# Kernel optimization log

Measured on AMD Instinct MI355X. Metric: run time of the kernel, lower is better.

## Reference

```python
import jax, jax.numpy as jnp
import numpy as np

B, S, W = 16, 256, 128            # batch, seq_len (word pieces), words per sentence
V, H, L, NH, DH, FF, C = 30522, 768, 12, 12, 64, 3072, 425
EPS = 1e-12                        # HF Bert LayerNorm eps


def setup_inputs() -> dict:
    key = jax.random.key(0)
    kiter = iter(jax.random.split(key, 64))
    nk = lambda: next(kiter)
    # each word maps to 1 or 2 word-pieces -> total pieces in [W, 2W] <= S
    word_piece_tracked = jax.random.randint(nk(), (B, W), 1, 3)
    lengths = jnp.sum(word_piece_tracked, axis=1)
    encoded_batch = jax.random.randint(nk(), (B, S), 0, V)
    mask = (jnp.arange(S)[None, :] < lengths[:, None]).astype(jnp.int32)
    p = lambda *shape: jax.random.normal(nk(), shape, jnp.float32) * 0.02
    return dict(
        encoded_batch=encoded_batch, mask=mask, word_piece_tracked=word_piece_tracked,
        word_emb=p(V, H), pos_emb=p(S, H), type_emb=p(1, H),
        emb_ln_s=jnp.ones((H,), jnp.float32), emb_ln_b=jnp.zeros((H,), jnp.float32),
        Wq=p(L, H, H), bq=p(L, H), Wk=p(L, H, H), bk=p(L, H),
        Wv=p(L, H, H), bv=p(L, H), Wo=p(L, H, H), bo=p(L, H),
        ln1_s=jnp.ones((L, H), jnp.float32), ln1_b=jnp.zeros((L, H), jnp.float32),
        Wi=p(L, H, FF), bi=p(L, FF), Wo2=p(L, FF, H), bo2=p(L, H),
        ln2_s=jnp.ones((L, H), jnp.float32), ln2_b=jnp.zeros((L, H), jnp.float32),
        w1=p(H, 1024), b1=p(1024), w2=p(1024, C), b2=p(C),
    )


def _layer_norm(x, s, b):
    mu = jnp.mean(x, -1, keepdims=True)
    var = jnp.var(x, -1, keepdims=True)
    return (x - mu) * jax.lax.rsqrt(var + EPS) * s + b


def _forward(encoded_batch, mask, word_piece_tracked,
             word_emb, pos_emb, type_emb, emb_ln_s, emb_ln_b,
             Wq, bq, Wk, bk, Wv, bv, Wo, bo, ln1_s, ln1_b,
             Wi, bi, Wo2, bo2, ln2_s, ln2_b, w1, b1, w2, b2):
    # BERT embeddings (token_type all zeros)
    x = word_emb[encoded_batch] + pos_emb[None, :, :] + type_emb[0]
    x = _layer_norm(x, emb_ln_s, emb_ln_b)
    attn_bias = (1.0 - mask.astype(jnp.float32))[:, None, None, :] * -10000.0
    scale = 1.0 / np.sqrt(DH).astype(np.float32)

    def step(h, lp):
        wq, bq_, wk, bk_, wv, bv_, wo, bo_, l1s, l1b, wi, bi_, wo2, bo2_, l2s, l2b = lp
        q = (h @ wq + bq_).reshape(B, S, NH, DH)
        k = (h @ wk + bk_).reshape(B, S, NH, DH)
        v = (h @ wv + bv_).reshape(B, S, NH, DH)
        att = jax.nn.softmax(jnp.einsum('bqhd,bkhd->bhqk', q, k) * scale + attn_bias, axis=-1)
        ctx = jnp.einsum('bhqk,bkhd->bqhd', att, v).reshape(B, S, H)
        h = _layer_norm(h + ctx @ wo + bo_, l1s, l1b)
        ff = jax.nn.gelu(h @ wi + bi_, approximate=False)
        h = _layer_norm(h + ff @ wo2 + bo2_, l2s, l2b)
        return h, None

    x, _ = jax.lax.scan(step, x, (Wq, bq, Wk, bk, Wv, bv, Wo, bo, ln1_s, ln1_b,
                                  Wi, bi, Wo2, bo2, ln2_s, ln2_b))

    # MLP head (dropout = identity in eval)
    f1 = jax.nn.relu(x) @ w1 + b1          # [B, S, 1024]
    f2 = jax.nn.relu(f1) @ w2 + b2          # [B, S, C]

    # ragged segment-mean pooling over word pieces (equiv. to the python loop)
    cum = jnp.cumsum(word_piece_tracked, axis=1)                         # [B, W]
    seg = jax.vmap(lambda c: jnp.searchsorted(c, jnp.arange(S), side='right'))(cum)  # [B, S]
    sums = jax.vmap(lambda f, s: jax.ops.segment_sum(f, s, num_segments=W))(f2, seg)
    pooled = sums / word_piece_tracked[..., None].astype(f2.dtype)       # [B, W, C]
    out = jnp.concatenate([pooled, f2[:, W:, :]], axis=1)                # [B, S, C]
    return jax.nn.softmax(out, axis=2)


def reference(encoded_batch, mask, word_piece_tracked,
              word_emb, pos_emb, type_emb, emb_ln_s, emb_ln_b,
              Wq, bq, Wk, bk, Wv, bv, Wo, bo, ln1_s, ln1_b,
              Wi, bi, Wo2, bo2, ln2_s, ln2_b, w1, b1, w2, b2):
    return _forward(encoded_batch, mask, word_piece_tracked,
                    word_emb, pos_emb, type_emb, emb_ln_s, emb_ln_b,
                    Wq, bq, Wk, bk, Wv, bv, Wo, bo, ln1_s, ln1_b,
                    Wi, bi, Wo2, bo2, ln2_s, ln2_b, w1, b1, w2, b2)
```

## Files before the change

### kernel.cpp

```cpp
#include <hip/hip_runtime.h>
#include <math.h>

#define BB 16
#define SS 256
#define WW 128
#define HH 768
#define LL 12
#define NHH 12
#define DHH 64
#define FFD 3072
#define CC 425
#define NTOK (BB*SS)
#define QKVN (3*HH)

typedef __attribute__((ext_vector_type(8))) short bf16x8;
typedef __attribute__((ext_vector_type(4))) float f32x4;

__device__ __forceinline__ float bf2f(unsigned short u) {
    union { unsigned int i; float f; } z; z.i = ((unsigned int)u) << 16; return z.f;
}
__device__ __forceinline__ unsigned short f2bf(float f) {
    union { float f; unsigned int i; } z; z.f = f;
    unsigned int i = z.i;
    unsigned int r = (i + 0x7fffu + ((i >> 16) & 1u)) >> 16;
    return (unsigned short)r;
}

__device__ __forceinline__ void gload16(const void* g, void* l) {
    __builtin_amdgcn_global_load_lds((const __attribute__((address_space(1))) void*)g,
                                     (__attribute__((address_space(3))) void*)l, 16, 0, 0);
}

template<int BM, int BN, int ACT_A, int ACT_C>
__launch_bounds__(256)
__global__ void gemm_bt(const unsigned short* __restrict__ A,
                        const unsigned short* __restrict__ Bt,
                        const float* __restrict__ bias,
                        unsigned short* __restrict__ Cm,
                        int M, int N, int K, int ldC) {
    constexpr bool BIG = (BM == 128 && BN == 128);
    constexpr int FM = BIG ? 4 : BM / 32;
    constexpr int FN = BIG ? 4 : BN / 32;
    constexpr int ASZ = BM * 32, BSZ = BN * 32;
    __shared__ __align__(16) unsigned short lA[2 * ASZ];
    __shared__ __align__(16) unsigned short lB[2 * BSZ];
    const int tid = threadIdx.x, w = tid >> 6, l = tid & 63;

    const int gx = gridDim.x;
    const int nwg = gx * gridDim.y;
    const int orig = blockIdx.y * gx + blockIdx.x;
    const int q = nwg >> 3, r = nwg & 7, xc = orig & 7, o8 = orig >> 3;
    const int wg = (xc < r ? xc * (q + 1) : r * (q + 1) + (xc - r) * q) + o8;
    const int m0 = (wg / gx) * BM, n0 = (wg % gx) * BN;

    const int wr = BIG ? (w >> 1) * 64 : (w >> 1) * (BM / 2);
    const int wc = BIG ? (w & 1) * 64 : (w & 1) * (BN / 2);
    const int lr = l & 15, lk = (l >> 4) * 8;
    const int rsw = ((lr >> 1) & 3) << 4;
    const int lrow = l >> 2;
    const int gs = (l & 3) ^ ((lrow >> 1) & 3);

    f32x4 acc[FM][FN];
#pragma unroll
    for (int m = 0; m < FM; ++m)
#pragma unroll
        for (int n = 0; n < FN; ++n) acc[m][n] = (f32x4){0.f, 0.f, 0.f, 0.f};

    auto stage = [&](int k0, unsigned short* dA, unsigned short* dB) {
        if (ACT_A) {
#pragma unroll
            for (int i = 0; i < BM / 64; ++i) {
                int idx = i * 256 + tid, row = idx >> 2, s = idx & 3, g2 = s ^ ((row >> 1) & 3);
                uint4 av = *(const uint4*)(A + (size_t)(m0 + row) * K + k0 + g2 * 8);
                unsigned short* p = (unsigned short*)&av;
#pragma unroll
                for (int j = 0; j < 8; ++j) if (p[j] & 0x8000u) p[j] = 0;
                *(uint4*)((char*)dA + row * 64 + s * 16) = av;
            }
        } else {
#pragma unroll
            for (int it = 0; it < BM / 64; ++it) {
                int c = w * (BM / 64) + it;
                gload16(A + (size_t)(m0 + c * 16 + lrow) * K + k0 + gs * 8, dA + c * 512);
            }
        }
#pragma unroll
        for (int it = 0; it < BN / 64; ++it) {
            int c = w * (BN / 64) + it;
            gload16(Bt + (size_t)(n0 + c * 16 + lrow) * K + k0 + gs * 8, dB + c * 512);
        }
    };

    const int nt = K >> 5;
    stage(0, lA, lB);
    __syncthreads();

    for (int t = 0; t < nt; ++t) {
        unsigned short* cA = lA + (t & 1) * ASZ;
        unsigned short* cB = lB + (t & 1) * BSZ;
        if (t + 1 < nt)
            stage((t + 1) << 5, lA + ((t + 1) & 1) * ASZ, lB + ((t + 1) & 1) * BSZ);
        bf16x8 af[FM], bfr[FN];
#pragma unroll
        for (int m = 0; m < FM; ++m) {
            int row = wr + m * 16 + lr;
            af[m] = *(const bf16x8*)((const char*)cA + row * 64 + ((lk * 2) ^ rsw));
        }
#pragma unroll
        for (int n = 0; n < FN; ++n) {
            int row = wc + n * 16 + lr;
            bfr[n] = *(const bf16x8*)((const char*)cB + row * 64 + ((lk * 2) ^ rsw));
        }
#pragma unroll
        for (int m = 0; m < FM; ++m)
#pragma unroll
            for (int n = 0; n < FN; ++n)
                acc[m][n] = __builtin_amdgcn_mfma_f32_16x16x32_bf16(af[m], bfr[n], acc[m][n], 0, 0, 0);
        __syncthreads();
    }

    const int orow = (l >> 4) * 4, ocol = l & 15;
#pragma unroll
    for (int m = 0; m < FM; ++m)
#pragma unroll
        for (int n = 0; n < FN; ++n) {
            int c = n0 + wc + n * 16 + ocol;
            if (c >= N) continue;
            float bb = bias[c];
#pragma unroll
            for (int j = 0; j < 4; ++j) {
                int rr = m0 + wr + m * 16 + orow + j;
                float vv = acc[m][n][j] + bb;
                if (ACT_C == 1) vv = 0.5f * vv * (1.0f + erff(vv * 0.70710678118654752f));
                Cm[(size_t)rr * ldC + c] = f2bf(vv);
            }
        }
}

template<int ACT_A, int ACT_C>
__launch_bounds__(256)
__global__ void gemm_aw(const unsigned short* __restrict__ A,
                        const float* __restrict__ Wm,
                        const float* __restrict__ bias,
                        unsigned short* __restrict__ Cm,
                        int M, int N, int K, int ldC) {
    __shared__ __align__(16) unsigned short lA[64][40];
    __shared__ __align__(16) unsigned short lB[64][40];
    const int tid = threadIdx.x;
    const int m0 = blockIdx.y * 64;
    const int n0 = blockIdx.x * 64;
    const int w = tid >> 6, l = tid & 63;
    const int wr = (w >> 1) * 32, wc = (w & 1) * 32;
    const int lr = l & 15, lk = (l >> 4) * 8;

    f32x4 acc[2][2];
#pragma unroll
    for (int m = 0; m < 2; ++m)
#pragma unroll
        for (int n = 0; n < 2; ++n) acc[m][n] = (f32x4){0.f, 0.f, 0.f, 0.f};

    const int arow = tid >> 2, akc = (tid & 3) << 3;
    const int bkr = tid >> 3, bnc = (tid & 7) << 3;
    const bool nvec = (N & 7) == 0;

    for (int k0 = 0; k0 < K; k0 += 32) {
        uint4 av = *(const uint4*)(A + (size_t)(m0 + arow) * K + (k0 + akc));
        if (ACT_A) {
            unsigned short* p = (unsigned short*)&av;
#pragma unroll
            for (int j = 0; j < 8; ++j) if (p[j] & 0x8000u) p[j] = 0;
        }
        *(uint4*)&lA[arow][akc] = av;
        unsigned short bv[8];
        if (nvec) {
            const float* wp = Wm + (size_t)(k0 + bkr) * N + (n0 + bnc);
            float4 w0 = *(const float4*)(wp);
            float4 w1 = *(const float4*)(wp + 4);
            bv[0] = f2bf(w0.x); bv[1] = f2bf(w0.y); bv[2] = f2bf(w0.z); bv[3] = f2bf(w0.w);
            bv[4] = f2bf(w1.x); bv[5] = f2bf(w1.y); bv[6] = f2bf(w1.z); bv[7] = f2bf(w1.w);
        } else {
#pragma unroll
            for (int j = 0; j < 8; ++j) {
                int col = n0 + bnc + j;
                bv[j] = (col < N) ? f2bf(Wm[(size_t)(k0 + bkr) * N + col]) : (unsigned short)0;
            }
        }
#pragma unroll
        for (int j = 0; j < 8; ++j) lB[bnc + j][bkr] = bv[j];
        __syncthreads();

        bf16x8 af[2], bfr[2];
#pragma unroll
        for (int m = 0; m < 2; ++m) af[m] = *(const bf16x8*)&lA[wr + m * 16 + lr][lk];
#pragma unroll
        for (int n = 0; n < 2; ++n) bfr[n] = *(const bf16x8*)&lB[wc + n * 16 + lr][lk];
#pragma unroll
        for (int m = 0; m < 2; ++m)
#pragma unroll
            for (int n = 0; n < 2; ++n)
                acc[m][n] = __builtin_amdgcn_mfma_f32_16x16x32_bf16(af[m], bfr[n], acc[m][n], 0, 0, 0);
        __syncthreads();
    }

    const int orow = (l >> 4) * 4, ocol = l & 15;
#pragma unroll
    for (int m = 0; m < 2; ++m)
#pragma unroll
        for (int n = 0; n < 2; ++n) {
            int c = n0 + wc + n * 16 + ocol;
            if (c >= N) continue;
            float bb = bias[c];
#pragma unroll
            for (int j = 0; j < 4; ++j) {
                int r = m0 + wr + m * 16 + orow + j;
                float vv = acc[m][n][j] + bb;
                if (ACT_C == 1) vv = 0.5f * vv * (1.0f + erff(vv * 0.70710678118654752f));
                Cm[(size_t)r * ldC + c] = f2bf(vv);
            }
        }
}

__global__ void transpose_w(const float* __restrict__ src, unsigned short* __restrict__ dst,
                            int K, int N, long srcLS, long dstLS) {
    int n0 = blockIdx.x * 32, k0 = blockIdx.y * 32;
    src += (size_t)blockIdx.z * srcLS;
    dst += (size_t)blockIdx.z * dstLS;
    __shared__ float tile[32][33];
    int tx = threadIdx.x & 31, ty = threadIdx.x >> 5;
#pragma unroll
    for (int r = 0; r < 4; ++r) {
        int k = k0 + ty + r * 8, n = n0 + tx;
        tile[ty + r * 8][tx] = (n < N && k < K) ? src[(size_t)k * N + n] : 0.f;
    }
    __syncthreads();
    int col2 = threadIdx.x & 15, rowb = threadIdx.x >> 4;
#pragma unroll
    for (int p = 0; p < 2; ++p) {
        int n = n0 + rowb + p * 16;
        unsigned int lo = f2bf(tile[col2 * 2][rowb + p * 16]);
        unsigned int hi = f2bf(tile[col2 * 2 + 1][rowb + p * 16]);
        *(unsigned int*)(dst + (size_t)n * K + k0 + col2 * 2) = lo | (hi << 16);
    }
}

__global__ void concat_bias(const float* bq, const float* bk, const float* bv, float* bqkv) {
    int i = blockIdx.x * 256 + threadIdx.x;
    if (i >= LL * QKVN) return;
    int lyr = i / QKVN, c = i % QKVN;
    float v = (c < HH) ? bq[lyr * HH + c] : (c < 2 * HH) ? bk[lyr * HH + c - HH] : bv[lyr * HH + c - 2 * HH];
    bqkv[i] = v;
}

__global__ void build_maskbias(const int* mask, float* mb) {
    int i = blockIdx.x * 256 + threadIdx.x;
    mb[i] = mask[i] ? 0.0f : -10000.0f;
}

__launch_bounds__(256)
__global__ void attention_mfma(const unsigned short* __restrict__ qkv,
                               const float* __restrict__ mb,
                               unsigned short* __restrict__ ctx) {
    const int qt = blockIdx.x, h = blockIdx.y, b = blockIdx.z;
    const int tid = threadIdx.x, w = tid >> 6, l = tid & 63;
    __shared__ __align__(16) unsigned short lK[SS * DHH];
    __shared__ __align__(16) unsigned short lVt[DHH * SS];
    const size_t tokbase = (size_t)b * SS * QKVN;

    {
        const unsigned short* kp = qkv + tokbase + (size_t)tid * QKVN + HH + h * DHH;
        const unsigned short* vp = kp + HH;
#pragma unroll
        for (int c = 0; c < 8; ++c) {
            uint4 kd = *(const uint4*)(kp + c * 8);
            *(uint4*)((char*)lK + ((tid * 128 + c * 16) ^ ((tid & 7) << 4))) = kd;
            uint4 vd = *(const uint4*)(vp + c * 8);
            const unsigned short* e = (const unsigned short*)&vd;
#pragma unroll
            for (int j = 0; j < 8; ++j) {
                int d = c * 8 + j;
                *(unsigned short*)((char*)lVt + ((d * 512 + tid * 2) ^ ((d & 7) << 4))) = e[j];
            }
        }
    }
    const int q0w = qt * 64 + w * 16;
    const unsigned short* qp = qkv + tokbase + (size_t)(q0w + (l & 15)) * QKVN + h * DHH + (l >> 4) * 8;
    bf16x8 aq0 = *(const bf16x8*)(qp);
    bf16x8 aq1 = *(const bf16x8*)(qp + 32);
    __syncthreads();

    f32x4 sc[16];
#pragma unroll
    for (int t = 0; t < 16; ++t) {
        int key = t * 16 + (l & 15);
        int base = key * 128;
        int sw = (key & 7) << 4;
        bf16x8 bk0 = *(const bf16x8*)((char*)lK + ((base + (l >> 4) * 16) ^ sw));
        bf16x8 bk1 = *(const bf16x8*)((char*)lK + ((base + 64 + (l >> 4) * 16) ^ sw));
        f32x4 a = (f32x4){0.f, 0.f, 0.f, 0.f};
        a = __builtin_amdgcn_mfma_f32_16x16x32_bf16(aq0, bk0, a, 0, 0, 0);
        a = __builtin_amdgcn_mfma_f32_16x16x32_bf16(aq1, bk1, a, 0, 0, 0);
        sc[t] = a;
    }
    const float* mbb = mb + b * SS;
    float mx[4] = {-3.0e38f, -3.0e38f, -3.0e38f, -3.0e38f};
#pragma unroll
    for (int t = 0; t < 16; ++t) {
        float mv = mbb[t * 16 + (l & 15)];
#pragma unroll
        for (int r = 0; r < 4; ++r) {
            float v = sc[t][r] * 0.125f + mv;
            sc[t][r] = v;
            mx[r] = fmaxf(mx[r], v);
        }
    }
#pragma unroll
    for (int m = 1; m <= 8; m <<= 1)
#pragma unroll
        for (int r = 0; r < 4; ++r) mx[r] = fmaxf(mx[r], __shfl_xor(mx[r], m));
    float sm[4] = {0.f, 0.f, 0.f, 0.f};
#pragma unroll
    for (int t = 0; t < 16; ++t)
#pragma unroll
        for (int r = 0; r < 4; ++r) {
            float e = __expf(sc[t][r] - mx[r]);
            sc[t][r] = e;
            sm[r] += e;
        }
#pragma unroll
    for (int m = 1; m <= 8; m <<= 1)
#pragma unroll
        for (int r = 0; r < 4; ++r) sm[r] += __shfl_xor(sm[r], m);
    float inv[4];
#pragma unroll
    for (int r = 0; r < 4; ++r) inv[r] = 1.0f / sm[r];

    __syncthreads();
    unsigned short* P = lK;
#pragma unroll
    for (int t = 0; t < 16; ++t)
#pragma unroll
        for (int r = 0; r < 4; ++r) {
            int prow = w * 16 + (l >> 4) * 4 + r;
            int pcol = t * 16 + (l & 15);
            *(unsigned short*)((char*)P + ((prow * 512 + pcol * 2) ^ ((prow & 7) << 4))) =
                f2bf(sc[t][r] * inv[r]);
        }
    __syncthreads();

    f32x4 o[4];
#pragma unroll
    for (int dt = 0; dt < 4; ++dt) o[dt] = (f32x4){0.f, 0.f, 0.f, 0.f};
#pragma unroll
    for (int kt = 0; kt < 8; ++kt) {
        int prow = w * 16 + (l & 15);
        int pkb = (kt * 32 + (l >> 4) * 8) * 2;
        bf16x8 pa = *(const bf16x8*)((char*)P + ((prow * 512 + pkb) ^ ((prow & 7) << 4)));
#pragma unroll
        for (int dt = 0; dt < 4; ++dt) {
            int d = dt * 16 + (l & 15);
            bf16x8 vb = *(const bf16x8*)((char*)lVt + ((d * 512 + pkb) ^ ((d & 7) << 4)));
            o[dt] = __builtin_amdgcn_mfma_f32_16x16x32_bf16(pa, vb, o[dt], 0, 0, 0);
        }
    }
#pragma unroll
    for (int dt = 0; dt < 4; ++dt)
#pragma unroll
        for (int r = 0; r < 4; ++r) {
            int q = qt * 64 + w * 16 + (l >> 4) * 4 + r;
            int d = dt * 16 + (l & 15);
            ctx[((size_t)(b * SS + q)) * HH + h * DHH + d] = f2bf(o[dt][r]);
        }
}

__global__ void embed_ln(const int* __restrict__ ids,
                         const float* __restrict__ we,
                         const float* __restrict__ pe,
                         const float* __restrict__ te,
                         const float* __restrict__ g,
                         const float* __restrict__ beta,
                         unsigned short* __restrict__ x) {
    int t = blockIdx.x, s = t % SS, tid = threadIdx.x;
    int id = ids[t];
    __shared__ float r1[256], r2[256];
    float e[3]; float sum = 0.f, sq = 0.f;
#pragma unroll
    for (int j = 0; j < 3; ++j) {
        int i = tid + j * 256;
        float v = we[(size_t)id * HH + i] + pe[(size_t)s * HH + i] + te[i];
        e[j] = v; sum += v; sq += v * v;
    }
    r1[tid] = sum; r2[tid] = sq; __syncthreads();
    for (int o = 128; o > 0; o >>= 1) {
        if (tid < o) { r1[tid] += r1[tid + o]; r2[tid] += r2[tid + o]; }
        __syncthreads();
    }
    float mu = r1[0] * (1.0f / HH);
    float var = fmaxf(r2[0] * (1.0f / HH) - mu * mu, 0.f);
    float rs = rsqrtf(var + 1e-12f);
#pragma unroll
    for (int j = 0; j < 3; ++j) {
        int i = tid + j * 256;
        x[(size_t)t * HH + i] = f2bf((e[j] - mu) * rs * g[i] + beta[i]);
    }
}

__launch_bounds__(256)
__global__ void add_ln(unsigned short* __restrict__ x,
                       const unsigned short* __restrict__ y,
                       const float* __restrict__ g,
                       const float* __restrict__ beta) {
    const int t = blockIdx.x * 4 + (threadIdx.x >> 6);
    const int l = threadIdx.x & 63;
    const size_t base = (size_t)t * HH;
    float v[12];
    float sum = 0.f, sq = 0.f;
#pragma unroll
    for (int j = 0; j < 3; ++j) {
        uint2 xa = *(const uint2*)(x + base + j * 256 + l * 4);
        uint2 ya = *(const uint2*)(y + base + j * 256 + l * 4);
        const unsigned short* xp = (const unsigned short*)&xa;
        const unsigned short* yp = (const unsigned short*)&ya;
#pragma unroll
        for (int e = 0; e < 4; ++e) {
            float vv = bf2f(xp[e]) + bf2f(yp[e]);
            v[j * 4 + e] = vv;
            sum += vv; sq += vv * vv;
        }
    }
#pragma unroll
    for (int m = 1; m < 64; m <<= 1) {
        sum += __shfl_xor(sum, m);
        sq += __shfl_xor(sq, m);
    }
    float mu = sum * (1.0f / HH);
    float var = fmaxf(sq * (1.0f / HH) - mu * mu, 0.f);
    float rs = rsqrtf(var + 1e-12f);
#pragma unroll
    for (int j = 0; j < 3; ++j) {
        float4 gg = *(const float4*)(g + j * 256 + l * 4);
        float4 bb = *(const float4*)(beta + j * 256 + l * 4);
        unsigned int o0 = f2bf((v[j * 4 + 0] - mu) * rs * gg.x + bb.x);
        unsigned int o1 = f2bf((v[j * 4 + 1] - mu) * rs * gg.y + bb.y);
        unsigned int o2 = f2bf((v[j * 4 + 2] - mu) * rs * gg.z + bb.z);
        unsigned int o3 = f2bf((v[j * 4 + 3] - mu) * rs * gg.w + bb.w);
        uint2 st = {o0 | (o1 << 16), o2 | (o3 << 16)};
        *(uint2*)(x + base + j * 256 + l * 4) = st;
    }
}

__global__ void cumsum_k(const int* __restrict__ wpt, int* __restrict__ cum) {
    int b = blockIdx.x, w = threadIdx.x;
    int s = 0;
    for (int j = 0; j <= w; ++j) s += wpt[b * WW + j];
    cum[b * WW + w] = s;
}

__global__ void pool_softmax(const unsigned short* __restrict__ f2,
                             const int* __restrict__ cum,
                             float* __restrict__ out) {
    int t = blockIdx.x, b = t / SS, s = t % SS, tid = threadIdx.x;
    __shared__ float red[512];
    float val = -1e30f;
    bool act = tid < CC;
    if (act) {
        if (s < WW) {
            int end = cum[b * WW + s];
            int start = s ? cum[b * WW + s - 1] : 0;
            float su = 0.f;
            for (int j = start; j < end; ++j) su += bf2f(f2[((size_t)b * SS + j) * CC + tid]);
            val = su / (float)(end - start);
        } else {
            val = bf2f(f2[((size_t)b * SS + s) * CC + tid]);
        }
    }
    red[tid] = val; __syncthreads();
    for (int o = 256; o > 0; o >>= 1) {
        if (tid < o) red[tid] = fmaxf(red[tid], red[tid + o]);
        __syncthreads();
    }
    float mx = red[0]; __syncthreads();
    float e = act ? expf(val - mx) : 0.f;
    red[tid] = e; __syncthreads();
    for (int o = 256; o > 0; o >>= 1) {
        if (tid < o) red[tid] += red[tid + o];
        __syncthreads();
    }
    float inv = 1.0f / red[0];
    if (act) out[((size_t)b * SS + s) * CC + tid] = e * inv;
}

static inline size_t al256(size_t x) { return (x + 255) & ~(size_t)255; }

extern "C" void kernel_launch(void* const* d_in, const int* in_sizes, int n_in,
                              void* d_out, int out_size, void* d_ws, size_t ws_size,
                              hipStream_t stream) {
    const int* enc   = (const int*)d_in[0];
    const int* mask  = (const int*)d_in[1];
    const int* wpt   = (const int*)d_in[2];
    const float* word_emb = (const float*)d_in[3];
    const float* pos_emb  = (const float*)d_in[4];
    const float* type_emb = (const float*)d_in[5];
    const float* eln_s = (const float*)d_in[6];
    const float* eln_b = (const float*)d_in[7];
    const float* Wq = (const float*)d_in[8];
    const float* bq = (const float*)d_in[9];
    const float* Wk = (const float*)d_in[10];
    const float* bk = (const float*)d_in[11];
    const float* Wv = (const float*)d_in[12];
    const float* bv = (const float*)d_in[13];
    const float* Wo = (const float*)d_in[14];
    const float* bo = (const float*)d_in[15];
    const float* ln1s = (const float*)d_in[16];
    const float* ln1b = (const float*)d_in[17];
    const float* Wi = (const float*)d_in[18];
    const float* bi = (const float*)d_in[19];
    const float* Wo2 = (const float*)d_in[20];
    const float* bo2 = (const float*)d_in[21];
    const float* ln2s = (const float*)d_in[22];
    const float* ln2b = (const float*)d_in[23];
    const float* w1 = (const float*)d_in[24];
    const float* b1 = (const float*)d_in[25];
    const float* w2 = (const float*)d_in[26];
    const float* b2 = (const float*)d_in[27];

    unsigned char* ws = (unsigned char*)d_ws;
    size_t off = 0;
    unsigned short* x    = (unsigned short*)(ws + off); off = al256(off + (size_t)NTOK * HH * 2);
    unsigned short* qkv  = (unsigned short*)(ws + off); off = al256(off + (size_t)NTOK * QKVN * 2);
    unsigned short* ctx  = (unsigned short*)(ws + off); off = al256(off + (size_t)NTOK * HH * 2);
    unsigned short* proj = (unsigned short*)(ws + off); off = al256(off + (size_t)NTOK * HH * 2);
    unsigned short* ff   = (unsigned short*)(ws + off); off = al256(off + (size_t)NTOK * FFD * 2);
    unsigned short* f1   = (unsigned short*)(ws + off); off = al256(off + (size_t)NTOK * 1024 * 2);
    unsigned short* f2   = (unsigned short*)(ws + off); off = al256(off + (size_t)NTOK * CC * 2);
    float* mb            = (float*)(ws + off);          off = al256(off + (size_t)NTOK * 4);
    int* cum             = (int*)(ws + off);            off = al256(off + (size_t)BB * WW * 4);
    float* bqkv          = (float*)(ws + off);          off = al256(off + (size_t)LL * QKVN * 4);
    size_t offFast = off;
    unsigned short* WqkvT = (unsigned short*)(ws + offFast); offFast = al256(offFast + (size_t)LL * QKVN * HH * 2);
    unsigned short* WoT   = (unsigned short*)(ws + offFast); offFast = al256(offFast + (size_t)LL * HH * HH * 2);
    unsigned short* WiT   = (unsigned short*)(ws + offFast); offFast = al256(offFast + (size_t)LL * FFD * HH * 2);
    unsigned short* Wo2T  = (unsigned short*)(ws + offFast); offFast = al256(offFast + (size_t)LL * HH * FFD * 2);
    unsigned short* w1T   = (unsigned short*)(ws + offFast); offFast = al256(offFast + (size_t)1024 * HH * 2);
    unsigned short* w2T   = (unsigned short*)(ws + offFast); offFast = al256(offFast + (size_t)512 * 1024 * 2);
    const bool fast = (ws_size >= offFast);

    build_maskbias<<<NTOK / 256, 256, 0, stream>>>(mask, mb);
    concat_bias<<<(LL * QKVN + 255) / 256, 256, 0, stream>>>(bq, bk, bv, bqkv);

    if (fast) {
        transpose_w<<<dim3(24, 24, LL), 256, 0, stream>>>(Wq, WqkvT, HH, HH, (long)HH * HH, (long)QKVN * HH);
        transpose_w<<<dim3(24, 24, LL), 256, 0, stream>>>(Wk, WqkvT + (size_t)HH * HH, HH, HH, (long)HH * HH, (long)QKVN * HH);
        transpose_w<<<dim3(24, 24, LL), 256, 0, stream>>>(Wv, WqkvT + (size_t)2 * HH * HH, HH, HH, (long)HH * HH, (long)QKVN * HH);
        transpose_w<<<dim3(24, 24, LL), 256, 0, stream>>>(Wo, WoT, HH, HH, (long)HH * HH, (long)HH * HH);
        transpose_w<<<dim3(96, 24, LL), 256, 0, stream>>>(Wi, WiT, HH, FFD, (long)HH * FFD, (long)FFD * HH);
        transpose_w<<<dim3(24, 96, LL), 256, 0, stream>>>(Wo2, Wo2T, FFD, HH, (long)FFD * HH, (long)HH * FFD);
        transpose_w<<<dim3(32, 24, 1), 256, 0, stream>>>(w1, w1T, HH, 1024, 0, 0);
        transpose_w<<<dim3(16, 32, 1), 256, 0, stream>>>(w2, w2T, 1024, CC, 0, 0);
    }

    embed_ln<<<NTOK, 256, 0, stream>>>(enc, word_emb, pos_emb, type_emb, eln_s, eln_b, x);

    const dim3 gQKV(QKVN / 128, NTOK / 128);
    const dim3 gWo(HH / 64, NTOK / 64);
    const dim3 gFF1(FFD / 128, NTOK / 128);
    const dim3 gFF2(HH / 64, NTOK / 64);
    const dim3 gH1(1024 / 128, NTOK / 64);
    const dim3 gH2(7, NTOK / 64);
    const dim3 gAttn(4, NHH, BB);

    for (int l = 0; l < LL; ++l) {
        if (fast) {
            gemm_bt<128, 128, 0, 0><<<gQKV, 256, 0, stream>>>(x, WqkvT + (size_t)l * QKVN * HH, bqkv + l * QKVN, qkv, NTOK, QKVN, HH, QKVN);
        } else {
            const dim3 g64(HH / 64, NTOK / 64);
            gemm_aw<0, 0><<<g64, 256, 0, stream>>>(x, Wq + (size_t)l * HH * HH, bq + l * HH, qkv, NTOK, HH, HH, QKVN);
            gemm_aw<0, 0><<<g64, 256, 0, stream>>>(x, Wk + (size_t)l * HH * HH, bk + l * HH, qkv + HH, NTOK, HH, HH, QKVN);
            gemm_aw<0, 0><<<g64, 256, 0, stream>>>(x, Wv + (size_t)l * HH * HH, bv + l * HH, qkv + 2 * HH, NTOK, HH, HH, QKVN);
        }
        attention_mfma<<<gAttn, 256, 0, stream>>>(qkv, mb, ctx);
        if (fast) {
            gemm_bt<64, 64, 0, 0><<<gWo, 256, 0, stream>>>(ctx, WoT + (size_t)l * HH * HH, bo + l * HH, proj, NTOK, HH, HH, HH);
        } else {
            gemm_aw<0, 0><<<dim3(HH / 64, NTOK / 64), 256, 0, stream>>>(ctx, Wo + (size_t)l * HH * HH, bo + l * HH, proj, NTOK, HH, HH, HH);
        }
        add_ln<<<NTOK / 4, 256, 0, stream>>>(x, proj, ln1s + l * HH, ln1b + l * HH);
        if (fast) {
            gemm_bt<128, 128, 0, 1><<<gFF1, 256, 0, stream>>>(x, WiT + (size_t)l * FFD * HH, bi + l * FFD, ff, NTOK, FFD, HH, FFD);
            gemm_bt<64, 64, 0, 0><<<gFF2, 256, 0, stream>>>(ff, Wo2T + (size_t)l * HH * FFD, bo2 + l * HH, proj, NTOK, HH, FFD, HH);
        } else {
            gemm_aw<0, 1><<<dim3(FFD / 64, NTOK / 64), 256, 0, stream>>>(x, Wi + (size_t)l * HH * FFD, bi + l * FFD, ff, NTOK, FFD, HH, FFD);
            gemm_aw<0, 0><<<dim3(HH / 64, NTOK / 64), 256, 0, stream>>>(ff, Wo2 + (size_t)l * FFD * HH, bo2 + l * HH, proj, NTOK, HH, FFD, HH);
        }
        add_ln<<<NTOK / 4, 256, 0, stream>>>(x, proj, ln2s + l * HH, ln2b + l * HH);
    }

    if (fast) {
        gemm_bt<64, 128, 1, 0><<<gH1, 256, 0, stream>>>(x, w1T, b1, f1, NTOK, 1024, HH, 1024);
        gemm_bt<64, 64, 1, 0><<<gH2, 256, 0, stream>>>(f1, w2T, b2, f2, NTOK, CC, 1024, CC);
    } else {
        gemm_aw<1, 0><<<dim3(1024 / 64, NTOK / 64), 256, 0, stream>>>(x, w1, b1, f1, NTOK, 1024, HH, 1024);
        gemm_aw<1, 0><<<dim3(7, NTOK / 64), 256, 0, stream>>>(f1, w2, b2, f2, NTOK, CC, 1024, CC);
    }
    cumsum_k<<<BB, WW, 0, stream>>>(wpt, cum);
    pool_softmax<<<NTOK, 512, 0, stream>>>(f2, cum, (float*)d_out);
}
```

Baseline: 2.188 ms.

## Triple-buffer GEMM LDS pipeline, use polynomial GELU, move ReLU to separate kernels

The bf16 GEMM moves from a double-buffered LDS loop with two barriers per K-step to a triple-buffered ring. It uses explicit vmcnt waits and one barrier per step, so global-to-LDS loads run two tiles ahead of the MFMA work. The erff-based GELU epilogue is replaced by an Abramowitz-Stegun polynomial with a fast exp, which cuts epilogue math cost in the FFN1 GEMM at a small accuracy cost. The fused ReLU-on-A staging path is removed: separate relu_bf16 kernels write ReLU'd copies of the activations before the head GEMMs. This lets the head GEMMs use async global_load_lds, at the cost of extra memory traffic and kernel launches.

```diff
diff --git a/kernel.cpp b/kernel.cpp
--- a/kernel.cpp
+++ b/kernel.cpp
@@ -31,7 +31,17 @@
                                      (__attribute__((address_space(3))) void*)l, 16, 0, 0);
 }
 
-template<int BM, int BN, int ACT_A, int ACT_C>
+__device__ __forceinline__ float gelu_f(float v) {
+    float ax = fabsf(v) * 0.70710678118654752f;
+    float t = 1.0f / fmaf(0.3275911f, ax, 1.0f);
+    float poly = t * fmaf(t, fmaf(t, fmaf(t, fmaf(t, 1.061405429f, -1.453152027f),
+                                          1.421413741f), -0.284496736f), 0.254829592f);
+    float er = 1.0f - poly * __expf(-ax * ax);
+    er = (v < 0.f) ? -er : er;
+    return 0.5f * v * (1.0f + er);
+}
+
+template<int BM, int BN, int ACT_C>
 __launch_bounds__(256)
 __global__ void gemm_bt(const unsigned short* __restrict__ A,
                         const unsigned short* __restrict__ Bt,
@@ -42,8 +52,9 @@
     constexpr int FM = BIG ? 4 : BM / 32;
     constexpr int FN = BIG ? 4 : BN / 32;
     constexpr int ASZ = BM * 32, BSZ = BN * 32;
-    __shared__ __align__(16) unsigned short lA[2 * ASZ];
-    __shared__ __align__(16) unsigned short lB[2 * BSZ];
+    constexpr int LDS_L = BM / 64 + BN / 64;
+    __shared__ __align__(16) unsigned short lA[3 * ASZ];
+    __shared__ __align__(16) unsigned short lB[3 * BSZ];
     const int tid = threadIdx.x, w = tid >> 6, l = tid & 63;
 
     const int gx = gridDim.x;
@@ -67,22 +78,10 @@
         for (int n = 0; n < FN; ++n) acc[m][n] = (f32x4){0.f, 0.f, 0.f, 0.f};
 
     auto stage = [&](int k0, unsigned short* dA, unsigned short* dB) {
-        if (ACT_A) {
-#pragma unroll
-            for (int i = 0; i < BM / 64; ++i) {
-                int idx = i * 256 + tid, row = idx >> 2, s = idx & 3, g2 = s ^ ((row >> 1) & 3);
-                uint4 av = *(const uint4*)(A + (size_t)(m0 + row) * K + k0 + g2 * 8);
-                unsigned short* p = (unsigned short*)&av;
-#pragma unroll
-                for (int j = 0; j < 8; ++j) if (p[j] & 0x8000u) p[j] = 0;
-                *(uint4*)((char*)dA + row * 64 + s * 16) = av;
-            }
-        } else {
-#pragma unroll
-            for (int it = 0; it < BM / 64; ++it) {
-                int c = w * (BM / 64) + it;
-                gload16(A + (size_t)(m0 + c * 16 + lrow) * K + k0 + gs * 8, dA + c * 512);
-            }
+#pragma unroll
+        for (int it = 0; it < BM / 64; ++it) {
+            int c = w * (BM / 64) + it;
+            gload16(A + (size_t)(m0 + c * 16 + lrow) * K + k0 + gs * 8, dA + c * 512);
         }
 #pragma unroll
         for (int it = 0; it < BN / 64; ++it) {
@@ -92,31 +91,41 @@
     };
 
     const int nt = K >> 5;
-    stage(0, lA, lB);
-    __syncthreads();
+    unsigned short *a0 = lA, *a1 = lA + ASZ, *a2 = lA + 2 * ASZ;
+    unsigned short *b0 = lB, *b1 = lB + BSZ, *b2 = lB + 2 * BSZ;
+    stage(0, a0, b0);
+    if (nt > 1) stage(32, a1, b1);
 
     for (int t = 0; t < nt; ++t) {
-        unsigned short* cA = lA + (t & 1) * ASZ;
-        unsigned short* cB = lB + (t & 1) * BSZ;
-        if (t + 1 < nt)
-            stage((t + 1) << 5, lA + ((t + 1) & 1) * ASZ, lB + ((t + 1) & 1) * BSZ);
+        if (t < nt - 1) {
+            if constexpr (LDS_L == 2)      asm volatile("s_waitcnt vmcnt(2)" ::: "memory");
+            else if constexpr (LDS_L == 3) asm volatile("s_waitcnt vmcnt(3)" ::: "memory");
+            else                           asm volatile("s_waitcnt vmcnt(4)" ::: "memory");
+        } else {
+            asm volatile("s_waitcnt vmcnt(0)" ::: "memory");
+        }
+        __builtin_amdgcn_s_barrier();
+        if (t + 2 < nt) stage((t + 2) << 5, a2, b2);
+
         bf16x8 af[FM], bfr[FN];
 #pragma unroll
         for (int m = 0; m < FM; ++m) {
             int row = wr + m * 16 + lr;
-            af[m] = *(const bf16x8*)((const char*)cA + row * 64 + ((lk * 2) ^ rsw));
+            af[m] = *(const bf16x8*)((const char*)a0 + row * 64 + ((lk * 2) ^ rsw));
         }
 #pragma unroll
         for (int n = 0; n < FN; ++n) {
             int row = wc + n * 16 + lr;
-            bfr[n] = *(const bf16x8*)((const char*)cB + row * 64 + ((lk * 2) ^ rsw));
+            bfr[n] = *(const bf16x8*)((const char*)b0 + row * 64 + ((lk * 2) ^ rsw));
         }
 #pragma unroll
         for (int m = 0; m < FM; ++m)
 #pragma unroll
             for (int n = 0; n < FN; ++n)
                 acc[m][n] = __builtin_amdgcn_mfma_f32_16x16x32_bf16(af[m], bfr[n], acc[m][n], 0, 0, 0);
-        __syncthreads();
+
+        unsigned short* ta = a0; a0 = a1; a1 = a2; a2 = ta;
+        unsigned short* tb = b0; b0 = b1; b1 = b2; b2 = tb;
     }
 
     const int orow = (l >> 4) * 4, ocol = l & 15;
@@ -131,7 +140,7 @@
             for (int j = 0; j < 4; ++j) {
                 int rr = m0 + wr + m * 16 + orow + j;
                 float vv = acc[m][n][j] + bb;
-                if (ACT_C == 1) vv = 0.5f * vv * (1.0f + erff(vv * 0.70710678118654752f));
+                if (ACT_C == 1) vv = gelu_f(vv);
                 Cm[(size_t)rr * ldC + c] = f2bf(vv);
             }
         }
@@ -214,7 +223,7 @@
             for (int j = 0; j < 4; ++j) {
                 int r = m0 + wr + m * 16 + orow + j;
                 float vv = acc[m][n][j] + bb;
-                if (ACT_C == 1) vv = 0.5f * vv * (1.0f + erff(vv * 0.70710678118654752f));
+                if (ACT_C == 1) vv = gelu_f(vv);
                 Cm[(size_t)r * ldC + c] = f2bf(vv);
             }
         }
@@ -254,6 +263,17 @@
 __global__ void build_maskbias(const int* mask, float* mb) {
     int i = blockIdx.x * 256 + threadIdx.x;
     mb[i] = mask[i] ? 0.0f : -10000.0f;
+}
+
+__global__ void relu_bf16(const unsigned short* __restrict__ in,
+                          unsigned short* __restrict__ out, int n8) {
+    int i = blockIdx.x * 256 + threadIdx.x;
+    if (i >= n8) return;
+    uint4 v = ((const uint4*)in)[i];
+    unsigned short* p = (unsigned short*)&v;
+#pragma unroll
+    for (int j = 0; j < 8; ++j) if (p[j] & 0x8000u) p[j] = 0;
+    ((uint4*)out)[i] = v;
 }
 
 __launch_bounds__(256)
@@ -532,6 +552,8 @@
     unsigned short* ff   = (unsigned short*)(ws + off); off = al256(off + (size_t)NTOK * FFD * 2);
     unsigned short* f1   = (unsigned short*)(ws + off); off = al256(off + (size_t)NTOK * 1024 * 2);
     unsigned short* f2   = (unsigned short*)(ws + off); off = al256(off + (size_t)NTOK * CC * 2);
+    unsigned short* xr   = (unsigned short*)(ws + off); off = al256(off + (size_t)NTOK * HH * 2);
+    unsigned short* f1r  = (unsigned short*)(ws + off); off = al256(off + (size_t)NTOK * 1024 * 2);
     float* mb            = (float*)(ws + off);          off = al256(off + (size_t)NTOK * 4);
     int* cum             = (int*)(ws + off);            off = al256(off + (size_t)BB * WW * 4);
     float* bqkv          = (float*)(ws + off);          off = al256(off + (size_t)LL * QKVN * 4);
@@ -564,13 +586,13 @@
     const dim3 gWo(HH / 64, NTOK / 64);
     const dim3 gFF1(FFD / 128, NTOK / 128);
     const dim3 gFF2(HH / 64, NTOK / 64);
-    const dim3 gH1(1024 / 128, NTOK / 64);
+    const dim3 gH1(1024 / 64, NTOK / 64);
     const dim3 gH2(7, NTOK / 64);
     const dim3 gAttn(4, NHH, BB);
 
     for (int l = 0; l < LL; ++l) {
         if (fast) {
-            gemm_bt<128, 128, 0, 0><<<gQKV, 256, 0, stream>>>(x, WqkvT + (size_t)l * QKVN * HH, bqkv + l * QKVN, qkv, NTOK, QKVN, HH, QKVN);
+            gemm_bt<128, 128, 0><<<gQKV, 256, 0, stream>>>(x, WqkvT + (size_t)l * QKVN * HH, bqkv + l * QKVN, qkv, NTOK, QKVN, HH, QKVN);
         } else {
             const dim3 g64(HH / 64, NTOK / 64);
             gemm_aw<0, 0><<<g64, 256, 0, stream>>>(x, Wq + (size_t)l * HH * HH, bq + l * HH, qkv, NTOK, HH, HH, QKVN);
@@ -579,14 +601,14 @@
         }
         attention_mfma<<<gAttn, 256, 0, stream>>>(qkv, mb, ctx);
         if (fast) {
-            gemm_bt<64, 64, 0, 0><<<gWo, 256, 0, stream>>>(ctx, WoT + (size_t)l * HH * HH, bo + l * HH, proj, NTOK, HH, HH, HH);
+            gemm_bt<64, 64, 0><<<gWo, 256, 0, stream>>>(ctx, WoT + (size_t)l * HH * HH, bo + l * HH, proj, NTOK, HH, HH, HH);
         } else {
             gemm_aw<0, 0><<<dim3(HH / 64, NTOK / 64), 256, 0, stream>>>(ctx, Wo + (size_t)l * HH * HH, bo + l * HH, proj, NTOK, HH, HH, HH);
         }
         add_ln<<<NTOK / 4, 256, 0, stream>>>(x, proj, ln1s + l * HH, ln1b + l * HH);
         if (fast) {
-            gemm_bt<128, 128, 0, 1><<<gFF1, 256, 0, stream>>>(x, WiT + (size_t)l * FFD * HH, bi + l * FFD, ff, NTOK, FFD, HH, FFD);
-            gemm_bt<64, 64, 0, 0><<<gFF2, 256, 0, stream>>>(ff, Wo2T + (size_t)l * HH * FFD, bo2 + l * HH, proj, NTOK, HH, FFD, HH);
+            gemm_bt<128, 128, 1><<<gFF1, 256, 0, stream>>>(x, WiT + (size_t)l * FFD * HH, bi + l * FFD, ff, NTOK, FFD, HH, FFD);
+            gemm_bt<64, 64, 0><<<gFF2, 256, 0, stream>>>(ff, Wo2T + (size_t)l * HH * FFD, bo2 + l * HH, proj, NTOK, HH, FFD, HH);
         } else {
             gemm_aw<0, 1><<<dim3(FFD / 64, NTOK / 64), 256, 0, stream>>>(x, Wi + (size_t)l * HH * FFD, bi + l * FFD, ff, NTOK, FFD, HH, FFD);
             gemm_aw<0, 0><<<dim3(HH / 64, NTOK / 64), 256, 0, stream>>>(ff, Wo2 + (size_t)l * FFD * HH, bo2 + l * HH, proj, NTOK, HH, FFD, HH);
@@ -594,12 +616,17 @@
         add_ln<<<NTOK / 4, 256, 0, stream>>>(x, proj, ln2s + l * HH, ln2b + l * HH);
     }
 
+    relu_bf16<<<(NTOK * HH / 8 + 255) / 256, 256, 0, stream>>>(x, xr, NTOK * HH / 8);
     if (fast) {
-        gemm_bt<64, 128, 1, 0><<<gH1, 256, 0, stream>>>(x, w1T, b1, f1, NTOK, 1024, HH, 1024);
-        gemm_bt<64, 64, 1, 0><<<gH2, 256, 0, stream>>>(f1, w2T, b2, f2, NTOK, CC, 1024, CC);
+        gemm_bt<64, 64, 0><<<gH1, 256, 0, stream>>>(xr, w1T, b1, f1, NTOK, 1024, HH, 1024);
     } else {
-        gemm_aw<1, 0><<<dim3(1024 / 64, NTOK / 64), 256, 0, stream>>>(x, w1, b1, f1, NTOK, 1024, HH, 1024);
-        gemm_aw<1, 0><<<dim3(7, NTOK / 64), 256, 0, stream>>>(f1, w2, b2, f2, NTOK, CC, 1024, CC);
+        gemm_aw<0, 0><<<dim3(1024 / 64, NTOK / 64), 256, 0, stream>>>(xr, w1, b1, f1, NTOK, 1024, HH, 1024);
+    }
+    relu_bf16<<<(NTOK * 1024 / 8 + 255) / 256, 256, 0, stream>>>(f1, f1r, NTOK * 1024 / 8);
+    if (fast) {
+        gemm_bt<64, 64, 0><<<gH2, 256, 0, stream>>>(f1r, w2T, b2, f2, NTOK, CC, 1024, CC);
+    } else {
+        gemm_aw<0, 0><<<dim3(7, NTOK / 64), 256, 0, stream>>>(f1r, w2, b2, f2, NTOK, CC, 1024, CC);
     }
     cumsum_k<<<BB, WW, 0, stream>>>(wpt, cum);
     pool_softmax<<<NTOK, 512, 0, stream>>>(f2, cum, (float*)d_out);
```

Result: slower. 2.253 ms (+3.0%).
